# Performance work log

Hardware: AMD Instinct MI355X
Metric: run time of the kernel (lower is better)

The kernel has to match this reference:

```python
import jax, jax.numpy as jnp
import numpy as np

SEQ, D_IN, D_OUT = 8192, 768, 128


def setup_inputs() -> dict:
    key = jax.random.key(0)
    k1, k2, k3, k4 = jax.random.split(key, 4)
    x = jax.random.normal(k1, (SEQ, D_IN), dtype=jnp.float32)
    # torch nn.Linear weights are stored as [d_out, d_in]
    scale = 1.0 / np.sqrt(D_IN)
    w_query = jax.random.normal(k2, (D_OUT, D_IN), dtype=jnp.float32) * scale
    w_key = jax.random.normal(k3, (D_OUT, D_IN), dtype=jnp.float32) * scale
    w_value = jax.random.normal(k4, (D_OUT, D_IN), dtype=jnp.float32) * scale
    return {"x": x, "w_query": w_query, "w_key": w_key, "w_value": w_value}


def reference(x, w_query, w_key, w_value):
    # Linear with bias=False: y = x @ W.T   (W is [d_out, d_in])
    q = x @ w_query.T                      # [N, d_out]
    k = x @ w_key.T                        # [N, d_out]
    v = x @ w_value.T                      # [N, d_out]
    inv_sqrt_d = 1.0 / jnp.sqrt(jnp.float32(k.shape[-1]))
    scores = (q @ k.T) * inv_sqrt_d        # [N, N] -- fully materialized, as in source
    weights = jax.nn.softmax(scores, axis=-1)
    return weights @ v                     # [N, d_out]
```

## Files before the change

kernel.cpp:

```cpp
#include <hip/hip_runtime.h>
#include <stdint.h>

#define SEQ 8192
#define DIN 768
#define DOUT 128

typedef __attribute__((ext_vector_type(8))) short short8;
typedef __attribute__((ext_vector_type(8))) unsigned short ushort8v;
typedef __attribute__((ext_vector_type(4))) float f32x4;

#define CEXPF (1.4426950408889634f * 0.08838834764831845f)

#if __has_builtin(__builtin_amdgcn_exp2f)
#define EXP2(x) __builtin_amdgcn_exp2f(x)
#else
#define EXP2(x) __builtin_exp2f(x)
#endif

__device__ __forceinline__ unsigned short f2bf(float f) {
  return (unsigned short)((__float_as_uint(f) + 0x8000u) >> 16);
}

__device__ __forceinline__ void gload_lds16(const void* g, void* l) {
  __builtin_amdgcn_global_load_lds(
      (const __attribute__((address_space(1))) void*)g,
      (__attribute__((address_space(3))) void*)l, 16, 0, 0);
}

__global__ void conv_kernel(const float* __restrict__ x,
                            const float* __restrict__ wq,
                            const float* __restrict__ wk,
                            const float* __restrict__ wv,
                            unsigned short* __restrict__ xb,
                            unsigned short* __restrict__ Wb) {
  int b = blockIdx.x;
  if (b < 6144) {
    int idx4 = (b * 256 + threadIdx.x) * 4;
    float4 v = *(const float4*)(x + idx4);
    ushort4 o;
    o.x = f2bf(v.x); o.y = f2bf(v.y); o.z = f2bf(v.z); o.w = f2bf(v.w);
    *(ushort4*)(xb + idx4) = o;
  } else {
    int idx4 = ((b - 6144) * 256 + threadIdx.x) * 4;
    int z = idx4 / (DOUT * DIN);
    int rem = idx4 - z * (DOUT * DIN);
    const float* src = (z == 0) ? wq : (z == 1) ? wk : wv;
    float4 v = *(const float4*)(src + rem);
    float sc = (z == 0) ? CEXPF : 1.0f;
    ushort4 o;
    o.x = f2bf(v.x * sc); o.y = f2bf(v.y * sc);
    o.z = f2bf(v.z * sc); o.w = f2bf(v.w * sc);
    *(ushort4*)(Wb + idx4) = o;
  }
}

__launch_bounds__(256, 2)
__global__ void qkv_kernel(const unsigned short* __restrict__ xb,
                           const unsigned short* __restrict__ Wb,
                           unsigned short* __restrict__ Qb,
                           unsigned short* __restrict__ Kb,
                           unsigned short* __restrict__ Vtb) {
  __shared__ unsigned char lds[65536];

  const int t    = threadIdx.x;
  const int wave = t >> 6;
  const int lane = t & 63;
  const int g    = lane >> 4;
  const int r    = lane & 15;
  const int z    = blockIdx.y;
  const int m0   = blockIdx.x * 128;
  const unsigned short* Wz = Wb + (size_t)z * DOUT * DIN;

  auto stage = [&](int buf, int kb) {
    unsigned char* xs = lds + buf * 32768;
    unsigned char* ws = xs + 16384;
#pragma unroll
    for (int c = 0; c < 4; c++) {
      int ci  = (wave * 4 + c) * 64 + lane;
      int row = ci >> 3, ch = ci & 7;
      int sc  = (ch ^ (row & 7)) << 3;
      gload_lds16(xb + (size_t)(m0 + row) * DIN + kb + sc,
                  xs + ((wave * 4 + c) << 10) + (lane << 4));
      gload_lds16(Wz + (size_t)row * DIN + kb + sc,
                  ws + ((wave * 4 + c) << 10) + (lane << 4));
    }
  };

  f32x4 acc[8][2];
#pragma unroll
  for (int mt = 0; mt < 8; mt++)
#pragma unroll
    for (int nt = 0; nt < 2; nt++) acc[mt][nt] = 0.f;

  stage(0, 0);
  asm volatile("s_waitcnt vmcnt(0)" ::: "memory");
  __builtin_amdgcn_s_barrier();
  asm volatile("" ::: "memory");

#pragma unroll 1
  for (int s = 0; s < 12; s++) {
    const int cur = s & 1;
    if (s < 11) stage(cur ^ 1, (s + 1) * 64);
    unsigned char* xs = lds + cur * 32768;
    unsigned char* ws = xs + 16384;
    __builtin_amdgcn_s_setprio(1);
#pragma unroll
    for (int kc = 0; kc < 2; kc++) {
      short8 bfr[2];
#pragma unroll
      for (int nt = 0; nt < 2; nt++) {
        int row = wave * 32 + nt * 16 + r;
        bfr[nt] = *(const short8*)(xs + row * 128 + (((kc * 4 + g) ^ (row & 7)) << 4));
      }
#pragma unroll
      for (int mt = 0; mt < 8; mt++) {
        int oc = mt * 16 + r;
        short8 afr = *(const short8*)(ws + oc * 128 + (((kc * 4 + g) ^ (oc & 7)) << 4));
        acc[mt][0] = __builtin_amdgcn_mfma_f32_16x16x32_bf16(afr, bfr[0], acc[mt][0], 0, 0, 0);
        acc[mt][1] = __builtin_amdgcn_mfma_f32_16x16x32_bf16(afr, bfr[1], acc[mt][1], 0, 0, 0);
      }
    }
    __builtin_amdgcn_s_setprio(0);
    asm volatile("s_waitcnt vmcnt(0)" ::: "memory");
    __builtin_amdgcn_s_barrier();
    asm volatile("" ::: "memory");
  }

  if (z < 2) {
    unsigned short* out = (z == 0) ? Qb : Kb;
#pragma unroll
    for (int mt = 0; mt < 8; mt++)
#pragma unroll
      for (int nt = 0; nt < 2; nt++) {
        ushort4 o;
        o.x = f2bf(acc[mt][nt][0]); o.y = f2bf(acc[mt][nt][1]);
        o.z = f2bf(acc[mt][nt][2]); o.w = f2bf(acc[mt][nt][3]);
        *(ushort4*)(out + (size_t)(m0 + wave * 32 + nt * 16 + r) * DOUT + mt * 16 + g * 4) = o;
      }
  } else {
    unsigned short* ct = (unsigned short*)(lds + wave * 8704);
#pragma unroll
    for (int mt = 0; mt < 8; mt++)
#pragma unroll
      for (int nt = 0; nt < 2; nt++) {
        ushort4 o;
        o.x = f2bf(acc[mt][nt][0]); o.y = f2bf(acc[mt][nt][1]);
        o.z = f2bf(acc[mt][nt][2]); o.w = f2bf(acc[mt][nt][3]);
        *(ushort4*)&ct[(nt * 16 + r) * 136 + mt * 16 + g * 4] = o;
      }
    __syncthreads();
#pragma unroll
    for (int pass = 0; pass < 8; pass++) {
      int col = pass * 16 + (lane >> 2);
      int ch  = lane & 3;
      ushort8v a;
#pragma unroll
      for (int i = 0; i < 8; i++) a[i] = ct[(ch * 8 + i) * 136 + col];
      *(ushort8v*)(Vtb + (size_t)col * SEQ + m0 + wave * 32 + ch * 8) = a;
    }
  }
}

__launch_bounds__(256, 2)
__global__ void attn_kernel(const unsigned short* __restrict__ Qb,
                            const unsigned short* __restrict__ Kb,
                            const unsigned short* __restrict__ Vtb,
                            float* __restrict__ Opart,
                            float* __restrict__ lpart) {
  __shared__ unsigned char lds[51200];
  unsigned char* Kl = lds;
  unsigned char* Vl = lds + 16384;

  const int t    = threadIdx.x;
  const int wave = t >> 6;
  const int lane = t & 63;
  const int g    = lane >> 4;
  const int r    = lane & 15;
  unsigned short* Pl = (unsigned short*)(lds + 32768 + wave * 4608);

  const int qb = blockIdx.x;
  const int sp = blockIdx.y;
  const int q0 = qb * 128 + wave * 32;
  const int kvbase = sp * 1024;

  auto stageK = [&](int kv0) {
#pragma unroll
    for (int c = 0; c < 4; c++) {
      int idx = (wave * 4 + c) * 64 + lane;
      int krow = idx >> 4, kch = idx & 15;
      gload_lds16(Kb + ((size_t)(kv0 + krow) << 7) + ((kch ^ (krow & 15)) << 3),
                  Kl + ((wave * 4 + c) << 10) + (lane << 4));
    }
  };
  auto stageV = [&](int kv0) {
#pragma unroll
    for (int c = 0; c < 4; c++) {
      int idx = (wave * 4 + c) * 64 + lane;
      int d = idx >> 3, c2 = idx & 7;
      gload_lds16(Vtb + (size_t)d * SEQ + kv0 + ((c2 ^ (d & 7)) << 3),
                  Vl + ((wave * 4 + c) << 10) + (lane << 4));
    }
  };

  short8 qf[2][4];
#pragma unroll
  for (int nt = 0; nt < 2; nt++)
#pragma unroll
    for (int kc = 0; kc < 4; kc++)
      qf[nt][kc] = *(const short8*)(Qb + (size_t)(q0 + nt * 16 + r) * DOUT + kc * 32 + g * 8);

  short8 onesf;
#pragma unroll
  for (int j = 0; j < 8; j++) onesf[j] = (r == 0) ? (short)0x3F80 : (short)0;

  f32x4 oacc[2][8];
  f32x4 lacc[2];
#pragma unroll
  for (int st = 0; st < 2; st++) {
    lacc[st] = 0.f;
#pragma unroll
    for (int n = 0; n < 8; n++) oacc[st][n] = 0.f;
  }

  stageK(kvbase);
  stageV(kvbase);
  asm volatile("s_waitcnt vmcnt(0)" ::: "memory");
  __builtin_amdgcn_s_barrier();
  asm volatile("" ::: "memory");

#pragma unroll 1
  for (int it = 0; it < 16; it++) {
    f32x4 sf[4][2];
#pragma unroll
    for (int mt = 0; mt < 4; mt++)
#pragma unroll
      for (int nt = 0; nt < 2; nt++) sf[mt][nt] = 0.f;
    __builtin_amdgcn_s_setprio(1);
#pragma unroll
    for (int mt = 0; mt < 4; mt++) {
      int row = mt * 16 + r;
#pragma unroll
      for (int kc = 0; kc < 4; kc++) {
        short8 kf = *(const short8*)(Kl + row * 256 + (((kc * 4 + g) ^ (row & 15)) << 4));
        sf[mt][0] = __builtin_amdgcn_mfma_f32_16x16x32_bf16(kf, qf[0][kc], sf[mt][0], 0, 0, 0);
        sf[mt][1] = __builtin_amdgcn_mfma_f32_16x16x32_bf16(kf, qf[1][kc], sf[mt][1], 0, 0, 0);
      }
    }
    __builtin_amdgcn_s_setprio(0);

#pragma unroll
    for (int mt = 0; mt < 4; mt++)
#pragma unroll
      for (int nt = 0; nt < 2; nt++) {
        ushort4 p;
        p.x = f2bf(EXP2(sf[mt][nt][0]));
        p.y = f2bf(EXP2(sf[mt][nt][1]));
        p.z = f2bf(EXP2(sf[mt][nt][2]));
        p.w = f2bf(EXP2(sf[mt][nt][3]));
        *(ushort4*)(Pl + (nt * 16 + r) * 72 + mt * 16 + g * 4) = p;
      }
    short8 pf[2][2];
#pragma unroll
    for (int st = 0; st < 2; st++)
#pragma unroll
      for (int c2 = 0; c2 < 2; c2++)
        pf[st][c2] = *(const short8*)(Pl + (st * 16 + r) * 72 + c2 * 32 + g * 8);

    asm volatile("s_waitcnt vmcnt(0)" ::: "memory");
    __builtin_amdgcn_s_barrier();
    asm volatile("" ::: "memory");
    if (it < 15) stageK(kvbase + (it + 1) * 64);

    __builtin_amdgcn_s_setprio(1);
#pragma unroll
    for (int nt = 0; nt < 8; nt++) {
      int d = nt * 16 + r;
#pragma unroll
      for (int c2 = 0; c2 < 2; c2++) {
        short8 vf = *(const short8*)(Vl + d * 128 + (((c2 * 4 + g) ^ (d & 7)) << 4));
        oacc[0][nt] = __builtin_amdgcn_mfma_f32_16x16x32_bf16(pf[0][c2], vf, oacc[0][nt], 0, 0, 0);
        oacc[1][nt] = __builtin_amdgcn_mfma_f32_16x16x32_bf16(pf[1][c2], vf, oacc[1][nt], 0, 0, 0);
      }
    }
#pragma unroll
    for (int st = 0; st < 2; st++) {
      lacc[st] = __builtin_amdgcn_mfma_f32_16x16x32_bf16(pf[st][0], onesf, lacc[st], 0, 0, 0);
      lacc[st] = __builtin_amdgcn_mfma_f32_16x16x32_bf16(pf[st][1], onesf, lacc[st], 0, 0, 0);
    }
    __builtin_amdgcn_s_setprio(0);

    asm volatile("" ::: "memory");
    __builtin_amdgcn_s_barrier();
    asm volatile("" ::: "memory");
    if (it < 15) {
      stageV(kvbase + (it + 1) * 64);
      asm volatile("s_waitcnt vmcnt(4)" ::: "memory");
      __builtin_amdgcn_s_barrier();
      asm volatile("" ::: "memory");
    }
  }

  const size_t pbase = (size_t)sp * SEQ;
#pragma unroll
  for (int st = 0; st < 2; st++)
#pragma unroll
    for (int rr = 0; rr < 4; rr++) {
      int qrow = q0 + st * 16 + g * 4 + rr;
#pragma unroll
      for (int nt = 0; nt < 8; nt++)
        Opart[(pbase + qrow) * DOUT + nt * 16 + r] = oacc[st][nt][rr];
      if (r == 0) lpart[pbase + qrow] = lacc[st][rr];
    }
}

__global__ void combine_kernel(const float* __restrict__ Opart,
                               const float* __restrict__ lpart,
                               float* __restrict__ out) {
  int idx = blockIdx.x * 256 + threadIdx.x;
  int s   = idx >> 5;
  int d4  = (idx & 31) * 4;
  float L = 0.f;
  f32x4 acc = 0.f;
#pragma unroll
  for (int p = 0; p < 8; p++) {
    L += lpart[p * SEQ + s];
    acc += *(const f32x4*)(Opart + ((size_t)p * SEQ + s) * DOUT + d4);
  }
  f32x4 res = acc * (1.0f / L);
  *(f32x4*)(out + (size_t)s * DOUT + d4) = res;
}

extern "C" void kernel_launch(void* const* d_in, const int* in_sizes, int n_in,
                              void* d_out, int out_size, void* d_ws, size_t ws_size,
                              hipStream_t stream) {
  const float* x  = (const float*)d_in[0];
  const float* wq = (const float*)d_in[1];
  const float* wk = (const float*)d_in[2];
  const float* wv = (const float*)d_in[3];
  float* out = (float*)d_out;

  unsigned short* Qb  = (unsigned short*)d_ws;
  unsigned short* Kb  = Qb + (size_t)SEQ * DOUT;
  unsigned short* Vtb = Kb + (size_t)SEQ * DOUT;
  float* Opart = (float*)(Vtb + (size_t)SEQ * DOUT);
  float* lpart = Opart + (size_t)8 * SEQ * DOUT;
  unsigned short* Wb  = (unsigned short*)Opart;
  unsigned short* xb  = Wb + (size_t)3 * DOUT * DIN;
  if (ws_size < (size_t)(6291456 + 33554432 + 262144)) return;

  conv_kernel<<<dim3(6432), 256, 0, stream>>>(x, wq, wk, wv, xb, Wb);
  qkv_kernel<<<dim3(64, 3), 256, 0, stream>>>(xb, Wb, Qb, Kb, Vtb);
  attn_kernel<<<dim3(64, 8), 256, 0, stream>>>(Qb, Kb, Vtb, Opart, lpart);
  combine_kernel<<<dim3(1024), 256, 0, stream>>>(Opart, lpart, out);
}
```

Measured before the change: 133.0 us.

## Double-buffer K/V tiles in LDS and use one barrier per iteration

K and V tiles move into two LDS buffers each. The next tile's K and V are prefetched at the start of every iteration while the current buffer is consumed, which cuts the per-iteration barriers from up to three to one. The per-wave P scratch shrinks by processing the two query sub-tiles one after another through the same buffer. Total LDS grows to about 73 KB per block, which still allows two blocks per CU but leaves less headroom.

```diff
diff --git a/kernel.cpp b/kernel.cpp
--- a/kernel.cpp
+++ b/kernel.cpp
@@ -167,23 +167,22 @@
                             const unsigned short* __restrict__ Vtb,
                             float* __restrict__ Opart,
                             float* __restrict__ lpart) {
-  __shared__ unsigned char lds[51200];
-  unsigned char* Kl = lds;
-  unsigned char* Vl = lds + 16384;
+  __shared__ unsigned char lds[74752];
 
   const int t    = threadIdx.x;
   const int wave = t >> 6;
   const int lane = t & 63;
   const int g    = lane >> 4;
   const int r    = lane & 15;
-  unsigned short* Pl = (unsigned short*)(lds + 32768 + wave * 4608);
+  unsigned short* Pl = (unsigned short*)(lds + 65536 + wave * 2304);
 
   const int qb = blockIdx.x;
   const int sp = blockIdx.y;
   const int q0 = qb * 128 + wave * 32;
   const int kvbase = sp * 1024;
 
-  auto stageK = [&](int kv0) {
+  auto stageK = [&](int buf, int kv0) {
+    unsigned char* Kl = lds + buf * 16384;
 #pragma unroll
     for (int c = 0; c < 4; c++) {
       int idx = (wave * 4 + c) * 64 + lane;
@@ -192,7 +191,8 @@
                   Kl + ((wave * 4 + c) << 10) + (lane << 4));
     }
   };
-  auto stageV = [&](int kv0) {
+  auto stageV = [&](int buf, int kv0) {
+    unsigned char* Vl = lds + 32768 + buf * 16384;
 #pragma unroll
     for (int c = 0; c < 4; c++) {
       int idx = (wave * 4 + c) * 64 + lane;
@@ -222,14 +222,22 @@
     for (int n = 0; n < 8; n++) oacc[st][n] = 0.f;
   }
 
-  stageK(kvbase);
-  stageV(kvbase);
+  stageK(0, kvbase);
+  stageV(0, kvbase);
   asm volatile("s_waitcnt vmcnt(0)" ::: "memory");
   __builtin_amdgcn_s_barrier();
   asm volatile("" ::: "memory");
 
 #pragma unroll 1
   for (int it = 0; it < 16; it++) {
+    const int cur = it & 1;
+    if (it < 15) {
+      stageK(cur ^ 1, kvbase + (it + 1) * 64);
+      stageV(cur ^ 1, kvbase + (it + 1) * 64);
+    }
+    unsigned char* Kl = lds + cur * 16384;
+    unsigned char* Vl = lds + 32768 + cur * 16384;
+
     f32x4 sf[4][2];
 #pragma unroll
     for (int mt = 0; mt < 4; mt++)
@@ -248,28 +256,22 @@
     }
     __builtin_amdgcn_s_setprio(0);
 
-#pragma unroll
-    for (int mt = 0; mt < 4; mt++)
-#pragma unroll
-      for (int nt = 0; nt < 2; nt++) {
+    short8 pf[2][2];
+#pragma unroll
+    for (int st = 0; st < 2; st++) {
+#pragma unroll
+      for (int mt = 0; mt < 4; mt++) {
         ushort4 p;
-        p.x = f2bf(EXP2(sf[mt][nt][0]));
-        p.y = f2bf(EXP2(sf[mt][nt][1]));
-        p.z = f2bf(EXP2(sf[mt][nt][2]));
-        p.w = f2bf(EXP2(sf[mt][nt][3]));
-        *(ushort4*)(Pl + (nt * 16 + r) * 72 + mt * 16 + g * 4) = p;
-      }
-    short8 pf[2][2];
-#pragma unroll
-    for (int st = 0; st < 2; st++)
+        p.x = f2bf(EXP2(sf[mt][st][0]));
+        p.y = f2bf(EXP2(sf[mt][st][1]));
+        p.z = f2bf(EXP2(sf[mt][st][2]));
+        p.w = f2bf(EXP2(sf[mt][st][3]));
+        *(ushort4*)(Pl + r * 72 + mt * 16 + g * 4) = p;
+      }
 #pragma unroll
       for (int c2 = 0; c2 < 2; c2++)
-        pf[st][c2] = *(const short8*)(Pl + (st * 16 + r) * 72 + c2 * 32 + g * 8);
-
-    asm volatile("s_waitcnt vmcnt(0)" ::: "memory");
-    __builtin_amdgcn_s_barrier();
-    asm volatile("" ::: "memory");
-    if (it < 15) stageK(kvbase + (it + 1) * 64);
+        pf[st][c2] = *(const short8*)(Pl + r * 72 + c2 * 32 + g * 8);
+    }
 
     __builtin_amdgcn_s_setprio(1);
 #pragma unroll
@@ -289,15 +291,9 @@
     }
     __builtin_amdgcn_s_setprio(0);
 
-    asm volatile("" ::: "memory");
+    asm volatile("s_waitcnt vmcnt(0)" ::: "memory");
     __builtin_amdgcn_s_barrier();
     asm volatile("" ::: "memory");
-    if (it < 15) {
-      stageV(kvbase + (it + 1) * 64);
-      asm volatile("s_waitcnt vmcnt(4)" ::: "memory");
-      __builtin_amdgcn_s_barrier();
-      asm volatile("" ::: "memory");
-    }
   }
 
   const size_t pbase = (size_t)sp * SEQ;
```

Result: no change. 133.2 us (+0.1%).
